# Kernel optimization log

Hardware: AMD Instinct MI355X
Metric: run time of the kernel (lower is better)

## Reference

```python
import jax, jax.numpy as jnp
import numpy as np

B, N, D, H = 4, 16384, 64, 8
MIN_FREQ = 1.0 / 64.0
SCALE = 1.0
EPS = 1e-5


def layernorm(x):
    # LayerNorm over last (head-feature) dim, no affine, biased variance (torch default)
    m = jnp.mean(x, axis=-1, keepdims=True)
    v = jnp.mean(jnp.square(x - m), axis=-1, keepdims=True)
    return (x - m) * jax.lax.rsqrt(v + EPS)


def rope_freqs(pos):
    # pos: [b, n, 1] 1-D coordinates -> freqs [b, n, D]
    inv_freq = 1.0 / (10000.0 ** (jnp.arange(0, D, 2, dtype=jnp.float32) / D))  # [D/2]
    t = pos[..., 0] * (SCALE / MIN_FREQ)                                         # [b, n]
    f = t[..., None] * inv_freq                                                  # [b, n, D/2]
    return jnp.concatenate([f, f], axis=-1)                                      # [b, n, D]


def rotate_half(x):
    x1, x2 = jnp.split(x, 2, axis=-1)
    return jnp.concatenate([-x2, x1], axis=-1)


def apply_rope(x, freqs):
    # x: [b, h, n, d], freqs: [b, n, d]
    c = jnp.cos(freqs)[:, None]
    s = jnp.sin(freqs)[:, None]
    return x * c + rotate_half(x) * s


def setup_inputs() -> dict:
    key = jax.random.key(0)
    ks = jax.random.split(key, 6)
    gain = 1.0 / D
    return {
        "x": jax.random.normal(ks[0], (B, N, D), dtype=jnp.float32),
        "pos": jax.random.uniform(ks[1], (B, N, 1), dtype=jnp.float32),
        "Wq": jax.random.normal(ks[2], (D, D * H), dtype=jnp.float32) * gain,
        "Wk": jax.random.normal(ks[3], (D, D * H), dtype=jnp.float32) * gain,
        "Wv": jax.random.normal(ks[4], (D, D * H), dtype=jnp.float32) * gain,
        "Wo": jax.random.normal(ks[5], (D * H, D), dtype=jnp.float32) * gain,
    }


def reference(x, pos, Wq, Wk, Wv, Wo):
    b, n, _ = x.shape

    def proj(W):
        # [b, n, d] @ [d, h*d] -> [b, h, n, d]
        y = jnp.einsum("bnd,de->bne", x, W)
        return y.reshape(b, n, H, D).transpose(0, 2, 1, 3)

    q, k, v = proj(Wq), proj(Wk), proj(Wv)

    # galerkin: layernorm k and v (no mask path)
    k = layernorm(k)
    v = layernorm(v)

    # RoPE on q, k
    freqs = rope_freqs(pos)
    q = apply_rope(q, freqs)
    k = apply_rope(k, freqs)

    # linear attention: z = q @ (k^T v) / n
    kv = jnp.einsum("bhnd,bhne->bhde", k, v)          # [b, h, d, d]
    z = jnp.einsum("bhnd,bhde->bhne", q, kv) / n      # [b, h, n, d]
    z = z.transpose(0, 2, 1, 3).reshape(b, n, H * D)  # [b, n, h*d]

    return jnp.einsum("bne,ed->bnd", z, Wo)           # out_proj (dropout=0)
```

## Files before the change

kernel.cpp:

```cpp
#include <hip/hip_runtime.h>

#define B_ 4
#define N_ 16384
#define D_ 64
#define H_ 8
#define E_ 512
#define NCHUNK 32
#define NTILES (N_ / 64)

typedef __attribute__((ext_vector_type(8))) short short8;
typedef __attribute__((ext_vector_type(4))) float f32x4;
typedef __attribute__((ext_vector_type(2))) unsigned int uint32x2;

__device__ __forceinline__ unsigned short f2b(float f) {
    unsigned u = __float_as_uint(f);
    return (unsigned short)((u + 0x7fffu + ((u >> 16) & 1u)) >> 16);
}
__device__ __forceinline__ float b2f(unsigned short u) {
    return __uint_as_float((unsigned)u << 16);
}

__device__ __forceinline__ unsigned cvtpk(float a, float b) {
    unsigned r;
    asm("v_cvt_pk_bf16_f32 %0, %1, %2" : "=v"(r) : "v"(a), "v"(b));
    return r;
}

template<int CTRL>
__device__ __forceinline__ float dppadd(float x) {
    int y = __builtin_amdgcn_update_dpp(0, __float_as_int(x), CTRL, 0xF, 0xF, true);
    return x + __int_as_float(y);
}
__device__ __forceinline__ float rowsum16(float x) {
    x = dppadd<0xB1>(x);
    x = dppadd<0x4E>(x);
    x = dppadd<0x141>(x);
    x = dppadd<0x140>(x);
    return x;
}

__global__ __launch_bounds__(256) void k_prep(
    const float* __restrict__ x,
    const float* __restrict__ Wq, const float* __restrict__ Wk,
    const float* __restrict__ Wv,
    unsigned short* __restrict__ WqB, unsigned short* __restrict__ WkB,
    unsigned short* __restrict__ WvB,
    unsigned short* __restrict__ CsB,
    unsigned short* __restrict__ xblob)
{
    const int bid = blockIdx.x, tid = threadIdx.x;
    if (bid < 384) {
        int mat = bid >> 7, sub = bid & 127;
        const float* src = (mat == 0) ? Wq : (mat == 1) ? Wk : Wv;
        unsigned short* dst = (mat == 0) ? WqB : (mat == 1) ? WkB : WvB;
        int id = sub * 256 + tid;
        int kin = id >> 9, f = id & 511;
        int h = f >> 6, feat = f & 63;
        int nt = feat >> 4, cc = feat & 15;
        int half = kin >> 5, qd = (kin >> 3) & 3, e = kin & 7;
        dst[(size_t)h * 4096 + (((nt * 2 + half) * 64 + qd * 16 + cc) * 8) + e]
            = f2b(src[id]);
        return;
    }
    if (bid < 2432) {
        int idx = (bid - 384) * 256 + tid;
        int lane = idx & 63, fr = (idx >> 6) & 1, tb = (idx >> 7) & 1023, b = idx >> 17;
        int cc = lane & 15, qd = lane >> 4;
        const float* src = &x[((size_t)b * N_ + tb * 16 + cc) * 64 + fr * 32 + qd * 8];
        float4 v0 = *(const float4*)src;
        float4 v1 = *(const float4*)(src + 4);
        ushort4 u0, u1;
        u0.x = f2b(v0.x); u0.y = f2b(v0.y); u0.z = f2b(v0.z); u0.w = f2b(v0.w);
        u1.x = f2b(v1.x); u1.y = f2b(v1.y); u1.z = f2b(v1.z); u1.w = f2b(v1.w);
        *(ushort4*)&xblob[(size_t)idx * 8]     = u0;
        *(ushort4*)&xblob[(size_t)idx * 8 + 4] = u1;
        return;
    }
    int idx = (bid - 2432) * 256 + tid;
    int h = idx >> 10, rem = idx & 1023;
    int half = rem >> 9, lane = (rem >> 3) & 63, e = rem & 7;
    int cc = lane & 15, qd = lane >> 4;
    int kin = half * 32 + qd * 8 + e;
    unsigned short outv = 0;
    if (cc < 2) {
        const float* Wsrc = (cc == 0) ? Wk : Wv;
        float acc = 0.f;
        #pragma unroll 8
        for (int f = 0; f < 64; ++f)
            acc += b2f(f2b(Wsrc[(size_t)kin * E_ + h * 64 + f]));
        outv = f2b(acc);
    }
    CsB[h * 1024 + half * 512 + lane * 8 + e] = outv;
}

__global__ __launch_bounds__(256, 4) void k_kv(
    const unsigned short* __restrict__ xblob,
    const float* __restrict__ pos,
    const unsigned short* __restrict__ WkB,
    const unsigned short* __restrict__ WvB,
    const unsigned short* __restrict__ CsB,
    float* __restrict__ kv_part)
{
    const int b = blockIdx.z, h = blockIdx.y, chunk = blockIdx.x;
    const int tid  = threadIdx.x;
    const int lane = tid & 63;
    const int w    = tid >> 6;
    const int c    = lane & 15;
    const int quad = lane >> 4;
    const int m0   = w * 16;

    __shared__ unsigned short kbuf[64 * 72];
    __shared__ unsigned short vbuf[64 * 72];
    __shared__ unsigned short wkl[4096];
    __shared__ unsigned short wvl[4096];
    __shared__ unsigned short wsl[1024];

    {
        const float4* srcK = (const float4*)(WkB + (size_t)h * 4096);
        const float4* srcV = (const float4*)(WvB + (size_t)h * 4096);
        float4* dstK = (float4*)wkl;
        float4* dstV = (float4*)wvl;
        #pragma unroll
        for (int i = 0; i < 2; ++i) {
            dstK[tid + i * 256] = srcK[tid + i * 256];
            dstV[tid + i * 256] = srcV[tid + i * 256];
        }
        if (tid < 128)
            ((float4*)wsl)[tid] = ((const float4*)(CsB + (size_t)h * 1024))[tid];
    }

    const float invf_lo = exp2f(-0.4152410118609203f * (float)c);
    const float invf_hi = invf_lo * 0.01f;
    const int bp0 = (lane & 48) << 2;
    const int bp1 = bp0 + 4;

    f32x4 akv[4];
    #pragma unroll
    for (int nt = 0; nt < 4; ++nt) akv[nt] = (f32x4){0.f, 0.f, 0.f, 0.f};

    short8 a0, a1;
    float tp[4];
    {
        int tb = chunk * 4 + w;
        const unsigned short* xb = xblob + (size_t)((b * 1024 + tb) * 2) * 512 + lane * 8;
        a0 = *(const short8*)&xb[0];
        a1 = *(const short8*)&xb[512];
        #pragma unroll
        for (int r = 0; r < 4; ++r)
            tp[r] = pos[(size_t)b * N_ + chunk * 64 + m0 + quad * 4 + r] * 64.0f;
    }
    __syncthreads();

    short8 bs0 = *(const short8*)&wsl[lane * 8];
    short8 bs1 = *(const short8*)&wsl[512 + lane * 8];

    for (int tile = chunk; tile < NTILES; tile += NCHUNK) {
        f32x4 ak[4], av[4];
        #pragma unroll
        for (int nt = 0; nt < 4; ++nt) {
            short8 bk0 = *(const short8*)&wkl[(nt * 2 + 0) * 512 + lane * 8];
            short8 bk1 = *(const short8*)&wkl[(nt * 2 + 1) * 512 + lane * 8];
            f32x4 z = {0.f, 0.f, 0.f, 0.f};
            z = __builtin_amdgcn_mfma_f32_16x16x32_bf16(a0, bk0, z, 0, 0, 0);
            ak[nt] = __builtin_amdgcn_mfma_f32_16x16x32_bf16(a1, bk1, z, 0, 0, 0);
            short8 bv0 = *(const short8*)&wvl[(nt * 2 + 0) * 512 + lane * 8];
            short8 bv1 = *(const short8*)&wvl[(nt * 2 + 1) * 512 + lane * 8];
            f32x4 y = {0.f, 0.f, 0.f, 0.f};
            y = __builtin_amdgcn_mfma_f32_16x16x32_bf16(a0, bv0, y, 0, 0, 0);
            av[nt] = __builtin_amdgcn_mfma_f32_16x16x32_bf16(a1, bv1, y, 0, 0, 0);
        }

        f32x4 asum;
        {
            f32x4 zz = {0.f, 0.f, 0.f, 0.f};
            zz = __builtin_amdgcn_mfma_f32_16x16x32_bf16(a0, bs0, zz, 0, 0, 0);
            asum = __builtin_amdgcn_mfma_f32_16x16x32_bf16(a1, bs1, zz, 0, 0, 0);
        }

        float cl[4], sl[4], ch[4], sh[4];
        #pragma unroll
        for (int r = 0; r < 4; ++r) {
            float al = tp[r] * invf_lo, ah = tp[r] * invf_hi;
            cl[r] = __cosf(al); sl[r] = __sinf(al);
            ch[r] = __cosf(ah); sh[r] = __sinf(ah);
        }

        const int tn = tile + NCHUNK;
        if (tn < NTILES) {
            int tb = tn * 4 + w;
            const unsigned short* xb = xblob + (size_t)((b * 1024 + tb) * 2) * 512 + lane * 8;
            a0 = *(const short8*)&xb[0];
            a1 = *(const short8*)&xb[512];
            #pragma unroll
            for (int r = 0; r < 4; ++r)
                tp[r] = pos[(size_t)b * N_ + tn * 64 + m0 + quad * 4 + r] * 64.0f;
        }
        __builtin_amdgcn_sched_barrier(0);

        #pragma unroll
        for (int r = 0; r < 4; ++r) {
            float sk2 = ak[0][r]*ak[0][r] + ak[1][r]*ak[1][r] + ak[2][r]*ak[2][r] + ak[3][r]*ak[3][r];
            float sv2 = av[0][r]*av[0][r] + av[1][r]*av[1][r] + av[2][r]*av[2][r] + av[3][r]*av[3][r];
            sk2 = rowsum16(sk2);
            sv2 = rowsum16(sv2);
            float mk = __int_as_float(__builtin_amdgcn_ds_bpermute(bp0, __float_as_int(asum[r]))) * (1.0f / 64.0f);
            float mv = __int_as_float(__builtin_amdgcn_ds_bpermute(bp1, __float_as_int(asum[r]))) * (1.0f / 64.0f);
            float rk = rsqrtf(sk2 * (1.0f / 64.0f) - mk * mk + 1e-5f);
            float rv = rsqrtf(sv2 * (1.0f / 64.0f) - mv * mv + 1e-5f);
            #pragma unroll
            for (int nt = 0; nt < 4; ++nt) {
                ak[nt][r] = (ak[nt][r] - mk) * rk;
                av[nt][r] = (av[nt][r] - mv) * rv;
            }
        }

        #pragma unroll
        for (int r = 0; r < 4; ++r) {
            float lo0 = ak[0][r], hi0 = ak[2][r];
            ak[0][r] = lo0 * cl[r] - hi0 * sl[r];
            ak[2][r] = hi0 * cl[r] + lo0 * sl[r];
            float lo1 = ak[1][r], hi1 = ak[3][r];
            ak[1][r] = lo1 * ch[r] - hi1 * sh[r];
            ak[3][r] = hi1 * ch[r] + lo1 * sh[r];
        }

        __syncthreads();

        #pragma unroll
        for (int nt = 0; nt < 4; ++nt) {
            uint32x2 kk, vv;
            kk[0] = cvtpk(ak[nt][0], ak[nt][1]);
            kk[1] = cvtpk(ak[nt][2], ak[nt][3]);
            vv[0] = cvtpk(av[nt][0], av[nt][1]);
            vv[1] = cvtpk(av[nt][2], av[nt][3]);
            *(uint32x2*)&kbuf[(nt * 16 + c) * 72 + m0 + quad * 4] = kk;
            *(uint32x2*)&vbuf[(nt * 16 + c) * 72 + m0 + quad * 4] = vv;
        }
        __syncthreads();

        short8 ka0 = *(const short8*)&kbuf[(m0 + c) * 72 + quad * 8];
        short8 ka1 = *(const short8*)&kbuf[(m0 + c) * 72 + 32 + quad * 8];
        #pragma unroll
        for (int nt = 0; nt < 4; ++nt) {
            short8 vb0 = *(const short8*)&vbuf[(nt * 16 + c) * 72 + quad * 8];
            short8 vb1 = *(const short8*)&vbuf[(nt * 16 + c) * 72 + 32 + quad * 8];
            akv[nt] = __builtin_amdgcn_mfma_f32_16x16x32_bf16(ka0, vb0, akv[nt], 0, 0, 0);
            akv[nt] = __builtin_amdgcn_mfma_f32_16x16x32_bf16(ka1, vb1, akv[nt], 0, 0, 0);
        }
    }

    float* dst = kv_part + ((size_t)(b * H_ + h) * NCHUNK + chunk) * 4096;
    #pragma unroll
    for (int nt = 0; nt < 4; ++nt)
        #pragma unroll
        for (int r = 0; r < 4; ++r)
            dst[(size_t)(16 * w + quad * 4 + r) * 64 + nt * 16 + c] = akv[nt][r];
}

__global__ __launch_bounds__(256) void k_m(
    const float* __restrict__ kv_part,
    const float* __restrict__ Wo,
    unsigned short* __restrict__ MTB)
{
    const int h = blockIdx.x, b = blockIdx.y, s = blockIdx.z;
    const int tid = threadIdx.x;
    __shared__ float kvs[8 * 65];
    __shared__ float wos[64 * 68];

    const float* src = kv_part + (size_t)(b * H_ + h) * NCHUNK * 4096 + s * 512;
    #pragma unroll
    for (int k = 0; k < 2; ++k) {
        int idx = tid + k * 256;
        float ssum = 0.f;
        #pragma unroll 8
        for (int ch = 0; ch < NCHUNK; ++ch) ssum += src[(size_t)ch * 4096 + idx];
        kvs[(idx >> 6) * 65 + (idx & 63)] = ssum;
    }
    for (int i = tid; i < 1024; i += 256) {
        int dp = i >> 4, j4 = (i & 15) * 4;
        *(float4*)&wos[dp * 68 + j4] = *(const float4*)&Wo[(size_t)(h * 64 + dp) * 64 + j4];
    }
    __syncthreads();

    const float inv_n = 1.0f / (float)N_;
    unsigned short* dst = MTB + (size_t)(b * H_ + h) * 4096;
    const int half = s >> 2, qd = s & 3;
    #pragma unroll
    for (int k = 0; k < 2; ++k) {
        int idx = tid + k * 256;
        int dl = idx >> 6, j = idx & 63;
        float acc = 0.f;
        #pragma unroll 8
        for (int e = 0; e < 64; ++e)
            acc += kvs[dl * 65 + e] * wos[e * 68 + j];
        int nt = j >> 4, cc = j & 15;
        dst[(((nt * 2 + half) * 64 + qd * 16 + cc) * 8) + dl] = f2b(acc * inv_n);
    }
}

__global__ __launch_bounds__(256, 3) void k_out(
    const unsigned short* __restrict__ xblob,
    const float* __restrict__ pos,
    const unsigned short* __restrict__ WqB,
    const unsigned short* __restrict__ MTB,
    float* __restrict__ out)
{
    const int b = blockIdx.y;
    const int n0 = blockIdx.x * 64;
    const int tid  = threadIdx.x;
    const int lane = tid & 63;
    const int w    = tid >> 6;
    const int c    = lane & 15;
    const int quad = lane >> 4;
    const int m0   = w * 16;

    __shared__ unsigned short qbuf[64 * 72];

    const int tb = blockIdx.x * 4 + w;
    const unsigned short* xb = xblob + (size_t)((b * 1024 + tb) * 2) * 512 + lane * 8;
    short8 a0 = *(const short8*)&xb[0];
    short8 a1 = *(const short8*)&xb[512];

    const unsigned short* wq0 = WqB + (size_t)lane * 8;
    const unsigned short* mt0 = MTB + (size_t)(b * H_) * 4096 + (size_t)lane * 8;
    short8 W[8], Mt[8];
    #pragma unroll
    for (int fr = 0; fr < 8; ++fr) W[fr]  = *(const short8*)&wq0[fr * 512];
    #pragma unroll
    for (int fr = 0; fr < 8; ++fr) Mt[fr] = *(const short8*)&mt0[fr * 512];
    __builtin_amdgcn_sched_barrier(0);

    const float tpv = pos[(size_t)b * N_ + n0 + m0 + c] * 64.0f;
    const float invfq = exp2f(-0.4152410118609203f * (float)(quad * 4));
    float csl[4], snl[4], csh[4], snh[4];
    {
        const float Kr[4] = {1.0f, 0.74989420933246f, 0.56234132519035f, 0.42169650342858f};
        #pragma unroll
        for (int r = 0; r < 4; ++r) {
            float al = tpv * invfq * Kr[r];
            float ah = al * 0.01f;
            csl[r] = __cosf(al); snl[r] = __sinf(al);
            csh[r] = __cosf(ah); snh[r] = __sinf(ah);
        }
    }

    f32x4 oacc[4];
    #pragma unroll
    for (int nt = 0; nt < 4; ++nt) oacc[nt] = (f32x4){0.f, 0.f, 0.f, 0.f};

    #pragma unroll
    for (int h = 0; h < H_; ++h) {
        f32x4 aqT[4];
        #pragma unroll
        for (int ntf = 0; ntf < 4; ++ntf) {
            f32x4 z = {0.f, 0.f, 0.f, 0.f};
            z = __builtin_amdgcn_mfma_f32_16x16x32_bf16(W[ntf * 2 + 0], a0, z, 0, 0, 0);
            aqT[ntf] = __builtin_amdgcn_mfma_f32_16x16x32_bf16(W[ntf * 2 + 1], a1, z, 0, 0, 0);
        }

        if (h < H_ - 1) {
            #pragma unroll
            for (int fr = 0; fr < 8; ++fr)
                W[fr] = *(const short8*)&wq0[(size_t)(h + 1) * 4096 + fr * 512];
        }
        __builtin_amdgcn_sched_barrier(0);

        #pragma unroll
        for (int r = 0; r < 4; ++r) {
            float lo0 = aqT[0][r], hi0 = aqT[2][r];
            aqT[0][r] = lo0 * csl[r] - hi0 * snl[r];
            aqT[2][r] = hi0 * csl[r] + lo0 * snl[r];
            float lo1 = aqT[1][r], hi1 = aqT[3][r];
            aqT[1][r] = lo1 * csh[r] - hi1 * snh[r];
            aqT[3][r] = hi1 * csh[r] + lo1 * snh[r];
        }

        #pragma unroll
        for (int ntf = 0; ntf < 4; ++ntf) {
            uint32x2 qq;
            qq[0] = cvtpk(aqT[ntf][0], aqT[ntf][1]);
            qq[1] = cvtpk(aqT[ntf][2], aqT[ntf][3]);
            *(uint32x2*)&qbuf[(m0 + c) * 72 + ntf * 16 + quad * 4] = qq;
        }

        short8 qa0 = *(const short8*)&qbuf[(m0 + c) * 72 + quad * 8];
        short8 qa1 = *(const short8*)&qbuf[(m0 + c) * 72 + 32 + quad * 8];
        #pragma unroll
        for (int nt = 0; nt < 4; ++nt) {
            oacc[nt] = __builtin_amdgcn_mfma_f32_16x16x32_bf16(qa0, Mt[nt * 2 + 0], oacc[nt], 0, 0, 0);
            oacc[nt] = __builtin_amdgcn_mfma_f32_16x16x32_bf16(qa1, Mt[nt * 2 + 1], oacc[nt], 0, 0, 0);
        }

        if (h < H_ - 1) {
            #pragma unroll
            for (int fr = 0; fr < 8; ++fr)
                Mt[fr] = *(const short8*)&mt0[(size_t)(h + 1) * 4096 + fr * 512];
        }
        __builtin_amdgcn_sched_barrier(0);
    }

    #pragma unroll
    for (int nt = 0; nt < 4; ++nt)
        #pragma unroll
        for (int r = 0; r < 4; ++r)
            out[(size_t)(b * N_ + n0 + m0 + quad * 4 + r) * 64 + nt * 16 + c] = oacc[nt][r];
}

extern "C" void kernel_launch(void* const* d_in, const int* in_sizes, int n_in,
                              void* d_out, int out_size, void* d_ws, size_t ws_size,
                              hipStream_t stream)
{
    const float* x   = (const float*)d_in[0];
    const float* pos = (const float*)d_in[1];
    const float* Wq  = (const float*)d_in[2];
    const float* Wk  = (const float*)d_in[3];
    const float* Wv  = (const float*)d_in[4];
    const float* Wo  = (const float*)d_in[5];
    float* out = (float*)d_out;

    char* ws = (char*)d_ws;
    float* kv_part        = (float*)ws;
    unsigned short* MTB   = (unsigned short*)(ws + 16777216);
    unsigned short* WqB   = (unsigned short*)(ws + 17039360);
    unsigned short* WkB   = (unsigned short*)(ws + 17104896);
    unsigned short* WvB   = (unsigned short*)(ws + 17170432);
    unsigned short* CsB   = (unsigned short*)(ws + 17235968);
    unsigned short* xblob = (unsigned short*)(ws + 17252352);

    k_prep<<<dim3(2464), 256, 0, stream>>>(x, Wq, Wk, Wv,
                                           WqB, WkB, WvB, CsB, xblob);
    k_kv  <<<dim3(NCHUNK, H_, B_), 256, 0, stream>>>(xblob, pos, WkB, WvB, CsB, kv_part);
    k_m   <<<dim3(H_, B_, 8), 256, 0, stream>>>(kv_part, Wo, MTB);
    k_out <<<dim3(NTILES, B_), 256, 0, stream>>>(xblob, pos, WqB, MTB, out);
}
```

Before: 146.0 us.

## Process two tiles per iteration in k_kv and cut chunk count to 24

Restructures the k_kv main loop so each iteration projects two tiles before normalising them, letting the LayerNorm/RoPE of the second tile overlap the shared-memory pack and KV accumulation of the first, and prefetches the next pair of x fragments. NCHUNK drops from 32 to 24, giving 768 blocks (about three per CU on a 256-CU part) with launch bounds lowered to 3 waves-per-SIMD occupancy, and the partial-KV buffer and reduction in k_m shrink to match. The extra live accumulators raise register pressure, and the uneven tile count per chunk needs a tail path.

```diff
diff --git a/kernel.cpp b/kernel.cpp
--- a/kernel.cpp
+++ b/kernel.cpp
@@ -5,7 +5,8 @@
 #define D_ 64
 #define H_ 8
 #define E_ 512
-#define NCHUNK 32
+#define NCHUNK 24
+#define NPART 24
 #define NTILES (N_ / 64)
 
 typedef __attribute__((ext_vector_type(8))) short short8;
@@ -93,7 +94,7 @@
     CsB[h * 1024 + half * 512 + lane * 8 + e] = outv;
 }
 
-__global__ __launch_bounds__(256, 4) void k_kv(
+__global__ __launch_bounds__(256, 3) void k_kv(
     const unsigned short* __restrict__ xblob,
     const float* __restrict__ pos,
     const unsigned short* __restrict__ WkB,
@@ -118,12 +119,10 @@
     {
         const float4* srcK = (const float4*)(WkB + (size_t)h * 4096);
         const float4* srcV = (const float4*)(WvB + (size_t)h * 4096);
-        float4* dstK = (float4*)wkl;
-        float4* dstV = (float4*)wvl;
         #pragma unroll
         for (int i = 0; i < 2; ++i) {
-            dstK[tid + i * 256] = srcK[tid + i * 256];
-            dstV[tid + i * 256] = srcV[tid + i * 256];
+            ((float4*)wkl)[tid + i * 256] = srcK[tid + i * 256];
+            ((float4*)wvl)[tid + i * 256] = srcV[tid + i * 256];
         }
         if (tid < 128)
             ((float4*)wsl)[tid] = ((const float4*)(CsB + (size_t)h * 1024))[tid];
@@ -138,45 +137,49 @@
     #pragma unroll
     for (int nt = 0; nt < 4; ++nt) akv[nt] = (f32x4){0.f, 0.f, 0.f, 0.f};
 
-    short8 a0, a1;
-    float tp[4];
-    {
-        int tb = chunk * 4 + w;
-        const unsigned short* xb = xblob + (size_t)((b * 1024 + tb) * 2) * 512 + lane * 8;
-        a0 = *(const short8*)&xb[0];
-        a1 = *(const short8*)&xb[512];
+    auto ldfrag = [&](int tileIdx, short8& f0, short8& f1, float tp[4]) {
+        int tb = tileIdx * 4 + w;
+        const unsigned short* xp = xblob + (size_t)((b * 1024 + tb) * 2) * 512 + lane * 8;
+        f0 = *(const short8*)&xp[0];
+        f1 = *(const short8*)&xp[512];
         #pragma unroll
         for (int r = 0; r < 4; ++r)
-            tp[r] = pos[(size_t)b * N_ + chunk * 64 + m0 + quad * 4 + r] * 64.0f;
-    }
+            tp[r] = pos[(size_t)b * N_ + tileIdx * 64 + m0 + quad * 4 + r] * 64.0f;
+    };
+
+    const int ntile = (NTILES - 1 - chunk) / NCHUNK + 1;
+    const int npair = ntile >> 1;
+    const bool tail = (ntile & 1) != 0;
+
+    short8 fA0, fA1, fB0, fB1;
+    float tpA[4], tpB[4];
+    ldfrag(chunk, fA0, fA1, tpA);
+    ldfrag(chunk + NCHUNK, fB0, fB1, tpB);
     __syncthreads();
 
     short8 bs0 = *(const short8*)&wsl[lane * 8];
     short8 bs1 = *(const short8*)&wsl[512 + lane * 8];
 
-    for (int tile = chunk; tile < NTILES; tile += NCHUNK) {
-        f32x4 ak[4], av[4];
+    auto proj = [&](short8 f0, short8 f1, f32x4* ak, f32x4* av, f32x4& as) {
         #pragma unroll
         for (int nt = 0; nt < 4; ++nt) {
             short8 bk0 = *(const short8*)&wkl[(nt * 2 + 0) * 512 + lane * 8];
             short8 bk1 = *(const short8*)&wkl[(nt * 2 + 1) * 512 + lane * 8];
             f32x4 z = {0.f, 0.f, 0.f, 0.f};
-            z = __builtin_amdgcn_mfma_f32_16x16x32_bf16(a0, bk0, z, 0, 0, 0);
-            ak[nt] = __builtin_amdgcn_mfma_f32_16x16x32_bf16(a1, bk1, z, 0, 0, 0);
+            z = __builtin_amdgcn_mfma_f32_16x16x32_bf16(f0, bk0, z, 0, 0, 0);
+            ak[nt] = __builtin_amdgcn_mfma_f32_16x16x32_bf16(f1, bk1, z, 0, 0, 0);
             short8 bv0 = *(const short8*)&wvl[(nt * 2 + 0) * 512 + lane * 8];
             short8 bv1 = *(const short8*)&wvl[(nt * 2 + 1) * 512 + lane * 8];
             f32x4 y = {0.f, 0.f, 0.f, 0.f};
-            y = __builtin_amdgcn_mfma_f32_16x16x32_bf16(a0, bv0, y, 0, 0, 0);
-            av[nt] = __builtin_amdgcn_mfma_f32_16x16x32_bf16(a1, bv1, y, 0, 0, 0);
-        }
-
-        f32x4 asum;
-        {
-            f32x4 zz = {0.f, 0.f, 0.f, 0.f};
-            zz = __builtin_amdgcn_mfma_f32_16x16x32_bf16(a0, bs0, zz, 0, 0, 0);
-            asum = __builtin_amdgcn_mfma_f32_16x16x32_bf16(a1, bs1, zz, 0, 0, 0);
-        }
-
+            y = __builtin_amdgcn_mfma_f32_16x16x32_bf16(f0, bv0, y, 0, 0, 0);
+            av[nt] = __builtin_amdgcn_mfma_f32_16x16x32_bf16(f1, bv1, y, 0, 0, 0);
+        }
+        f32x4 zz = {0.f, 0.f, 0.f, 0.f};
+        zz = __builtin_amdgcn_mfma_f32_16x16x32_bf16(f0, bs0, zz, 0, 0, 0);
+        as = __builtin_amdgcn_mfma_f32_16x16x32_bf16(f1, bs1, zz, 0, 0, 0);
+    };
+
+    auto lnrope = [&](f32x4* ak, f32x4* av, const f32x4& as, const float tp[4]) {
         float cl[4], sl[4], ch[4], sh[4];
         #pragma unroll
         for (int r = 0; r < 4; ++r) {
@@ -184,27 +187,14 @@
             cl[r] = __cosf(al); sl[r] = __sinf(al);
             ch[r] = __cosf(ah); sh[r] = __sinf(ah);
         }
-
-        const int tn = tile + NCHUNK;
-        if (tn < NTILES) {
-            int tb = tn * 4 + w;
-            const unsigned short* xb = xblob + (size_t)((b * 1024 + tb) * 2) * 512 + lane * 8;
-            a0 = *(const short8*)&xb[0];
-            a1 = *(const short8*)&xb[512];
-            #pragma unroll
-            for (int r = 0; r < 4; ++r)
-                tp[r] = pos[(size_t)b * N_ + tn * 64 + m0 + quad * 4 + r] * 64.0f;
-        }
-        __builtin_amdgcn_sched_barrier(0);
-
         #pragma unroll
         for (int r = 0; r < 4; ++r) {
             float sk2 = ak[0][r]*ak[0][r] + ak[1][r]*ak[1][r] + ak[2][r]*ak[2][r] + ak[3][r]*ak[3][r];
             float sv2 = av[0][r]*av[0][r] + av[1][r]*av[1][r] + av[2][r]*av[2][r] + av[3][r]*av[3][r];
             sk2 = rowsum16(sk2);
             sv2 = rowsum16(sv2);
-            float mk = __int_as_float(__builtin_amdgcn_ds_bpermute(bp0, __float_as_int(asum[r]))) * (1.0f / 64.0f);
-            float mv = __int_as_float(__builtin_amdgcn_ds_bpermute(bp1, __float_as_int(asum[r]))) * (1.0f / 64.0f);
+            float mk = __int_as_float(__builtin_amdgcn_ds_bpermute(bp0, __float_as_int(as[r]))) * (1.0f / 64.0f);
+            float mv = __int_as_float(__builtin_amdgcn_ds_bpermute(bp1, __float_as_int(as[r]))) * (1.0f / 64.0f);
             float rk = rsqrtf(sk2 * (1.0f / 64.0f) - mk * mk + 1e-5f);
             float rv = rsqrtf(sv2 * (1.0f / 64.0f) - mv * mv + 1e-5f);
             #pragma unroll
@@ -213,7 +203,6 @@
                 av[nt][r] = (av[nt][r] - mv) * rv;
             }
         }
-
         #pragma unroll
         for (int r = 0; r < 4; ++r) {
             float lo0 = ak[0][r], hi0 = ak[2][r];
@@ -223,9 +212,9 @@
             ak[1][r] = lo1 * ch[r] - hi1 * sh[r];
             ak[3][r] = hi1 * ch[r] + lo1 * sh[r];
         }
-
-        __syncthreads();
-
+    };
+
+    auto packkv = [&](f32x4* ak, f32x4* av) {
         #pragma unroll
         for (int nt = 0; nt < 4; ++nt) {
             uint32x2 kk, vv;
@@ -236,8 +225,9 @@
             *(uint32x2*)&kbuf[(nt * 16 + c) * 72 + m0 + quad * 4] = kk;
             *(uint32x2*)&vbuf[(nt * 16 + c) * 72 + m0 + quad * 4] = vv;
         }
-        __syncthreads();
-
+    };
+
+    auto kvacc = [&]() {
         short8 ka0 = *(const short8*)&kbuf[(m0 + c) * 72 + quad * 8];
         short8 ka1 = *(const short8*)&kbuf[(m0 + c) * 72 + 32 + quad * 8];
         #pragma unroll
@@ -247,9 +237,49 @@
             akv[nt] = __builtin_amdgcn_mfma_f32_16x16x32_bf16(ka0, vb0, akv[nt], 0, 0, 0);
             akv[nt] = __builtin_amdgcn_mfma_f32_16x16x32_bf16(ka1, vb1, akv[nt], 0, 0, 0);
         }
-    }
-
-    float* dst = kv_part + ((size_t)(b * H_ + h) * NCHUNK + chunk) * 4096;
+    };
+
+    #pragma unroll 1
+    for (int j = 0; j < npair; ++j) {
+        f32x4 akA[4], avA[4], asA;
+        f32x4 akB[4], avB[4], asB;
+        proj(fA0, fA1, akA, avA, asA);
+        proj(fB0, fB1, akB, avB, asB);
+
+        lnrope(akA, avA, asA, tpA);
+
+        __syncthreads();
+        packkv(akA, avA);
+        __syncthreads();
+        kvacc();
+
+        lnrope(akB, avB, asB, tpB);
+
+        int i2 = 2 * j + 2;
+        if (i2 < ntile) {
+            ldfrag(chunk + i2 * NCHUNK, fA0, fA1, tpA);
+            if (i2 + 1 < ntile)
+                ldfrag(chunk + (i2 + 1) * NCHUNK, fB0, fB1, tpB);
+        }
+        __builtin_amdgcn_sched_barrier(0);
+
+        __syncthreads();
+        packkv(akB, avB);
+        __syncthreads();
+        kvacc();
+    }
+
+    if (tail) {
+        f32x4 akA[4], avA[4], asA;
+        proj(fA0, fA1, akA, avA, asA);
+        lnrope(akA, avA, asA, tpA);
+        __syncthreads();
+        packkv(akA, avA);
+        __syncthreads();
+        kvacc();
+    }
+
+    float* dst = kv_part + ((size_t)(b * H_ + h) * NPART + chunk) * 4096;
     #pragma unroll
     for (int nt = 0; nt < 4; ++nt)
         #pragma unroll
@@ -267,13 +297,13 @@
     __shared__ float kvs[8 * 65];
     __shared__ float wos[64 * 68];
 
-    const float* src = kv_part + (size_t)(b * H_ + h) * NCHUNK * 4096 + s * 512;
+    const float* src = kv_part + (size_t)(b * H_ + h) * NPART * 4096 + s * 512;
     #pragma unroll
     for (int k = 0; k < 2; ++k) {
         int idx = tid + k * 256;
         float ssum = 0.f;
-        #pragma unroll 8
-        for (int ch = 0; ch < NCHUNK; ++ch) ssum += src[(size_t)ch * 4096 + idx];
+        #pragma unroll 6
+        for (int ch = 0; ch < NPART; ++ch) ssum += src[(size_t)ch * 4096 + idx];
         kvs[(idx >> 6) * 65 + (idx & 63)] = ssum;
     }
     for (int i = tid; i < 1024; i += 256) {
@@ -420,12 +450,12 @@
 
     char* ws = (char*)d_ws;
     float* kv_part        = (float*)ws;
-    unsigned short* MTB   = (unsigned short*)(ws + 16777216);
-    unsigned short* WqB   = (unsigned short*)(ws + 17039360);
-    unsigned short* WkB   = (unsigned short*)(ws + 17104896);
-    unsigned short* WvB   = (unsigned short*)(ws + 17170432);
-    unsigned short* CsB   = (unsigned short*)(ws + 17235968);
-    unsigned short* xblob = (unsigned short*)(ws + 17252352);
+    unsigned short* MTB   = (unsigned short*)(ws + 12582912);
+    unsigned short* WqB   = (unsigned short*)(ws + 12845056);
+    unsigned short* WkB   = (unsigned short*)(ws + 12910592);
+    unsigned short* WvB   = (unsigned short*)(ws + 12976128);
+    unsigned short* CsB   = (unsigned short*)(ws + 13041664);
+    unsigned short* xblob = (unsigned short*)(ws + 13058048);
 
     k_prep<<<dim3(2464), 256, 0, stream>>>(x, Wq, Wk, Wv,
                                            WqB, WkB, WvB, CsB, xblob);
```

Result: slower. 150.8 us (+3.3%).
